# Optimization experiments

Hardware: AMD Instinct MI355X
Metric: run time of the kernel (lower is better)

## Reference

```python
import jax, jax.numpy as jnp
import numpy as np

B, T, E, H, V = 128, 400, 128, 128, 50000
H2, H4, H6 = 2 * H, 4 * H, 6 * H


def setup_inputs() -> dict:
    key = jax.random.key(0)
    ks = jax.random.split(key, 16)
    s = 0.05
    return dict(
        input_ids=jax.random.randint(ks[0], (B, 1), 0, V),
        pre_hidden=jax.random.normal(ks[1], (1, B, H2), jnp.float32),
        pre_cell=jax.random.normal(ks[2], (1, B, H2), jnp.float32),
        enc_outputs=jax.random.normal(ks[3], (B, T, H2), jnp.float32),
        source_input=jax.random.randint(ks[4], (B, T), 0, V),
        coverage=jax.random.uniform(ks[5], (B, 1, T), jnp.float32),
        emb_table=s * jax.random.normal(ks[6], (V, E), jnp.float32),
        w_ih=s * jax.random.normal(ks[7], (4 * H2, E), jnp.float32),
        w_hh=s * jax.random.normal(ks[8], (4 * H2, H2), jnp.float32),
        b_ih=jnp.zeros((4 * H2,), jnp.float32),
        b_hh=jnp.zeros((4 * H2,), jnp.float32),
        w_align=s * jax.random.normal(ks[9], (1, H6), jnp.float32),
        b_align=jnp.zeros((1,), jnp.float32),
        w_cov=s * jax.random.normal(ks[10], (H2, 1), jnp.float32),
        b_cov=jnp.zeros((H2,), jnp.float32),
        w_fc1=s * jax.random.normal(ks[11], (H4, H4), jnp.float32),
        b_fc1=jnp.zeros((H4,), jnp.float32),
        w_fc2=s * jax.random.normal(ks[12], (V, H4), jnp.float32),
        b_fc2=jnp.zeros((V,), jnp.float32),
        w_gen=s * jax.random.normal(ks[13], (1, H4 + E), jnp.float32),
        b_gen=jnp.zeros((1,), jnp.float32),
    )


def reference(input_ids, pre_hidden, pre_cell, enc_outputs, source_input, coverage,
              emb_table, w_ih, w_hh, b_ih, b_hh, w_align, b_align, w_cov, b_cov,
              w_fc1, b_fc1, w_fc2, b_fc2, w_gen, b_gen):
    # embedding lookup (flag=False path: no dropout)
    emb = emb_table[input_ids[:, 0]]                      # [B,E]
    # single-step LSTM (PyTorch gate order i,f,g,o; hidden size 2H)
    h0, c0 = pre_hidden[0], pre_cell[0]                   # [B,2H]
    gates = emb @ w_ih.T + b_ih + h0 @ w_hh.T + b_hh      # [B,8H]
    i, f, g, o = jnp.split(gates, 4, axis=-1)
    c = jax.nn.sigmoid(f) * c0 + jax.nn.sigmoid(i) * jnp.tanh(g)
    h = jax.nn.sigmoid(o) * jnp.tanh(c)                   # [B,2H]
    # coverage feature + attention over encoder steps
    cov_feat = coverage.transpose(0, 2, 1) @ w_cov.T + b_cov        # [B,T,2H]
    h_rep = jnp.broadcast_to(h[:, None, :], enc_outputs.shape)     # [B,T,2H]
    combine = jnp.concatenate([enc_outputs, h_rep, cov_feat], -1)  # [B,T,6H]
    scores = jnp.tanh(combine @ w_align.T + b_align)               # [B,T,1]
    attn = jax.nn.softmax(scores, axis=1)                          # [B,T,1]
    attn_bt = attn[:, :, 0]                                        # [B,T]
    cov_bt = coverage[:, 0, :]
    cov_loss = jnp.sum(jnp.minimum(attn_bt, cov_bt))
    new_cov = coverage + attn_bt[:, None, :]                       # [B,1,T]
    # context + vocab distribution
    context = jnp.einsum('bt,bte->be', attn_bt, enc_outputs)       # [B,2H]
    fc = jnp.tanh(jnp.concatenate([h, context], -1) @ w_fc1.T + b_fc1)
    pvocab = jax.nn.softmax(fc @ w_fc2.T + b_fc2, axis=1)          # [B,V]
    # copy distribution: fused batched scatter-add (replaces per-batch one-hot matmul loop)
    b_idx = jnp.arange(attn_bt.shape[0])[:, None]
    copy = jnp.zeros_like(pvocab).at[b_idx, source_input].add(attn_bt)
    # generation probability and mixture
    gen_in = jnp.concatenate([context, h, emb], -1)                # [B,4H+E]
    pgen = jax.nn.sigmoid(gen_in @ w_gen.T + b_gen)                # [B,1]
    out = pvocab * pgen + copy * (1.0 - pgen)
    return (out, h[None], c[None], attn_bt[:, None, :], copy, new_cov, cov_loss)
```

## Files before the change

kernel.cpp:

```cpp
#include <hip/hip_runtime.h>
#include <hip/hip_bf16.h>
#include <math.h>

#define B_  128
#define T_  400
#define E_  128
#define H2_ 256
#define H4_ 512
#define V_  50000
#define G4_ 1024
#define KACT 384

#define OFF_H       6400000
#define OFF_C       6432768
#define OFF_ATTN    6465536
#define OFF_COPY    6516736
#define OFF_NEWCOV 12916736
#define OFF_COVLOSS 12967936

#define WS_ACT   0
#define WS_GATES (WS_ACT + KACT*B_)
#define WS_HC    (WS_GATES + G4_*B_)
#define WS_FCB   (WS_HC + H4_*B_)
#define WS_SC    (WS_FCB + H4_*B_/2)
#define WS_ATTN  (WS_SC + B_*T_)
#define WS_CTXP  (WS_ATTN + B_*T_)
#define WS_SMP   (WS_CTXP + B_*8*H2_)
#define WS_HDOT  (WS_SMP + B_*8*2)
#define WS_COVP  (WS_HDOT + B_)
#define WS_PGEN  (WS_COVP + B_)
#define WS_MAX   (WS_PGEN + B_)
#define WS_INV   (WS_MAX + B_)
#define WS_AB    (WS_INV + B_)

typedef __attribute__((ext_vector_type(8))) short bf16x8;
typedef __attribute__((ext_vector_type(4))) float f32x4;
typedef __attribute__((ext_vector_type(16))) float f32x16;

__device__ inline float sigmoidf_(float x){ return 1.f/(1.f+__expf(-x)); }

__device__ inline short f2bf(float x){
  __hip_bfloat16 h = __float2bfloat16(x);
  return *reinterpret_cast<short*>(&h);
}

__device__ inline float blk_reduce_sum(float v, float* red){
  int t = threadIdx.x;
  red[t] = v; __syncthreads();
  for (int s = 128; s > 0; s >>= 1){ if (t < s) red[t] += red[t+s]; __syncthreads(); }
  float r = red[0]; __syncthreads(); return r;
}
__device__ inline float blk_reduce_max(float v, float* red){
  int t = threadIdx.x;
  red[t] = v; __syncthreads();
  for (int s = 128; s > 0; s >>= 1){ if (t < s) red[t] = fmaxf(red[t], red[t+s]); __syncthreads(); }
  float r = red[0]; __syncthreads(); return r;
}

__global__ __launch_bounds__(256) void k_zero(float* __restrict__ p){
  size_t i = ((size_t)blockIdx.x*256 + threadIdx.x)*4;
  if (i < (size_t)B_*V_)
    *(float4*)&p[i] = make_float4(0.f,0.f,0.f,0.f);
}

__global__ __launch_bounds__(256) void k_act(const int* __restrict__ ids,
    const float* __restrict__ pre_h, const float* __restrict__ emb_table,
    const float* __restrict__ w_align, const float* __restrict__ w_cov,
    const float* __restrict__ b_cov, float* __restrict__ act,
    float* __restrict__ ab){
  __shared__ float red[256];
  int t = threadIdx.x;
  int idx = blockIdx.x*256 + t;
  int k = idx >> 7, b = idx & 127;
  float v = (k < E_) ? emb_table[(size_t)ids[b]*E_ + k]
                     : pre_h[b*H2_ + (k - E_)];
  act[idx] = v;
  if (blockIdx.x == 0) {
    float wa = w_align[2*H2_ + t];
    float alpha = blk_reduce_sum(w_cov[t]*wa, red);
    float beta  = blk_reduce_sum(b_cov[t]*wa, red);
    if (t == 0) { ab[0] = alpha; ab[1] = beta; }
  }
}

__global__ __launch_bounds__(256) void k_gates(const float* __restrict__ act,
    const float* __restrict__ w_ih, const float* __restrict__ w_hh,
    const float* __restrict__ b_ih, const float* __restrict__ b_hh,
    float* __restrict__ gates){
  __shared__ float wt[8][KACT];
  int t = threadIdx.x; int j0 = blockIdx.x*8;
  for (int idx = t; idx < 8*KACT; idx += 256) {
    int r = idx / KACT, k = idx % KACT;
    int j = j0 + r;
    wt[r][k] = (k < E_) ? w_ih[j*E_ + k] : w_hh[j*H2_ + (k - E_)];
  }
  __syncthreads();
  int jq = t >> 7, b = t & 127;
  float acc[4] = {0.f,0.f,0.f,0.f};
  for (int k = 0; k < KACT; ++k) {
    float a = act[k*B_ + b];
    #pragma unroll
    for (int jj = 0; jj < 4; ++jj) acc[jj] += wt[jq*4+jj][k]*a;
  }
  #pragma unroll
  for (int jj = 0; jj < 4; ++jj) {
    int j = j0 + jq*4 + jj;
    gates[j*B_ + b] = acc[jj] + b_ih[j] + b_hh[j];
  }
}

__global__ __launch_bounds__(256) void k_lstm(const float* __restrict__ gates,
    const float* __restrict__ pre_c, const float* __restrict__ w_align,
    float* __restrict__ o_h, float* __restrict__ o_c,
    float* __restrict__ hc, float* __restrict__ hdot){
  __shared__ float red[256];
  int b = blockIdx.x, k = threadIdx.x;
  float i_ = gates[(0*H2_ + k)*B_ + b];
  float f_ = gates[(1*H2_ + k)*B_ + b];
  float g_ = gates[(2*H2_ + k)*B_ + b];
  float o_ = gates[(3*H2_ + k)*B_ + b];
  float c = sigmoidf_(f_)*pre_c[b*H2_ + k] + sigmoidf_(i_)*tanhf(g_);
  float h = sigmoidf_(o_)*tanhf(c);
  o_h[b*H2_ + k] = h;
  o_c[b*H2_ + k] = c;
  hc[k*B_ + b] = h;
  float s = blk_reduce_sum(h * w_align[H2_ + k], red);
  if (k == 0) hdot[b] = s;
}

__global__ __launch_bounds__(256) void k_scores(const float* __restrict__ enc,
    const float* __restrict__ cov, const float* __restrict__ w_align,
    const float* __restrict__ b_align, const float* __restrict__ hdot,
    const float* __restrict__ ab, float* __restrict__ sc){
  int b = blockIdx.y, c = blockIdx.x;
  int t = threadIdx.x, wave = t >> 6, lane = t & 63;
  float4 wa4 = *(const float4*)&w_align[lane*4];
  float hd = hdot[b], alpha = ab[0], beta = ab[1], ba = b_align[0];
  int t0 = c*50;
  for (int tt = t0 + wave; tt < t0 + 50; tt += 4) {
    const float4* ep = (const float4*)&enc[((size_t)b*T_ + tt)*H2_];
    float4 e4 = ep[lane];
    float d = e4.x*wa4.x + e4.y*wa4.y + e4.z*wa4.z + e4.w*wa4.w;
    #pragma unroll
    for (int m = 32; m >= 1; m >>= 1) d += __shfl_xor(d, m);
    if (lane == 0)
      sc[b*T_ + tt] = tanhf(d + hd + alpha*cov[b*T_ + tt] + beta + ba);
  }
}

__global__ __launch_bounds__(256) void k_soft(const float* __restrict__ sc_in,
    const float* __restrict__ cov, const int* __restrict__ src,
    float* __restrict__ o_attn, float* __restrict__ o_newcov,
    float* __restrict__ o_copy, float* __restrict__ covp,
    float* __restrict__ attn_ws){
  __shared__ float red[256];
  int b = blockIdx.x, t = threadIdx.x;
  float x1 = sc_in[b*T_ + t];
  float x2 = (t + 256 < T_) ? sc_in[b*T_ + t + 256] : -1e30f;
  float mx = blk_reduce_max(fmaxf(x1, x2), red);
  float e1 = __expf(x1 - mx);
  float e2 = (t + 256 < T_) ? __expf(x2 - mx) : 0.f;
  float sum = blk_reduce_sum(e1 + e2, red);
  float inv = 1.f/sum;
  float cl;
  {
    float a1 = e1*inv; float c1 = cov[b*T_ + t];
    attn_ws[b*T_ + t] = a1;
    o_attn[b*T_ + t] = a1;
    o_newcov[b*T_ + t] = c1 + a1;
    atomicAdd(&o_copy[(size_t)b*V_ + src[b*T_ + t]], a1);
    cl = fminf(a1, c1);
  }
  if (t + 256 < T_) {
    float a2 = e2*inv; float c2 = cov[b*T_ + t + 256];
    attn_ws[b*T_ + t + 256] = a2;
    o_attn[b*T_ + t + 256] = a2;
    o_newcov[b*T_ + t + 256] = c2 + a2;
    atomicAdd(&o_copy[(size_t)b*V_ + src[b*T_ + t + 256]], a2);
    cl += fminf(a2, c2);
  }
  float clsum = blk_reduce_sum(cl, red);
  if (t == 0) covp[b] = clsum;
}

__global__ __launch_bounds__(256) void k_ctx(const float* __restrict__ enc,
    const float* __restrict__ attn_ws, float* __restrict__ ctxp){
  __shared__ float a_s[50];
  int b = blockIdx.y, c = blockIdx.x, e = threadIdx.x;
  int t0 = c*50;
  if (e < 50) a_s[e] = attn_ws[b*T_ + t0 + e];
  __syncthreads();
  float acc = 0.f;
  #pragma unroll 5
  for (int i = 0; i < 50; ++i)
    acc += a_s[i] * enc[((size_t)b*T_ + t0 + i)*H2_ + e];
  ctxp[((size_t)b*8 + c)*H2_ + e] = acc;
}

__global__ __launch_bounds__(256) void k_ctxpgen(const float* __restrict__ ctxp,
    const int* __restrict__ ids, const float* __restrict__ emb_table,
    const float* __restrict__ w_gen, const float* __restrict__ b_gen,
    float* __restrict__ hc, float* __restrict__ pgen){
  __shared__ float red[256];
  int b = blockIdx.x, t = threadIdx.x;
  float ctx = 0.f;
  #pragma unroll
  for (int c = 0; c < 8; ++c) ctx += ctxp[((size_t)b*8 + c)*H2_ + t];
  hc[(H2_ + t)*B_ + b] = ctx;
  float p = ctx*w_gen[t] + hc[t*B_ + b]*w_gen[H2_ + t];
  if (t < E_) p += emb_table[(size_t)ids[b]*E_ + t]*w_gen[2*H2_ + t];
  float s = blk_reduce_sum(p, red);
  if (t == 0) pgen[b] = sigmoidf_(s + b_gen[0]);
}

__global__ __launch_bounds__(256) void k_fc1(const float* __restrict__ hc,
    const float* __restrict__ w_fc1, const float* __restrict__ b_fc1,
    short* __restrict__ fcb){
  __shared__ float wt[16][H4_];
  int t = threadIdx.x; int j0 = blockIdx.x*16;
  for (int idx = t; idx < 16*H4_; idx += 256) {
    int r = idx >> 9, k = idx & 511;
    wt[r][k] = w_fc1[(j0 + r)*H4_ + k];
  }
  __syncthreads();
  int jq = t >> 7, b = t & 127;
  float acc[8] = {};
  for (int k = 0; k < H4_; ++k) {
    float a = hc[k*B_ + b];
    #pragma unroll
    for (int jj = 0; jj < 8; ++jj) acc[jj] += wt[jq*8+jj][k]*a;
  }
  bf16x8 pack;
  #pragma unroll
  for (int jj = 0; jj < 8; ++jj) {
    int j = j0 + jq*8 + jj;
    pack[jj] = f2bf(tanhf(acc[jj] + b_fc1[j]));
  }
  *(bf16x8*)&fcb[(size_t)b*H4_ + j0 + jq*8] = pack;
}

#define KH 256
__global__ __launch_bounds__(256, 2) void k_gemm2m(const short* __restrict__ fcb,
    const float* __restrict__ w_fc2, const float* __restrict__ b_fc2,
    float* __restrict__ logits){
  __shared__ short lds[B_*KH];
  char* ldsb = (char*)lds;
  int t = threadIdx.x;
  int w = t >> 6, l = t & 63;
  int ln = l & 31, g2 = l >> 5;
  int v = blockIdx.x*128 + w*32 + ln;
  int vc = v < V_ ? v : V_ - 1;
  f32x16 acc0 = {}, acc1 = {}, acc2 = {}, acc3 = {};

  #pragma unroll
  for (int h = 0; h < 2; ++h) {
    int kb = h*KH;
    if (h) __syncthreads();
    #pragma unroll
    for (int r = 0; r < 16; ++r) {
      int lid = r*256 + t;
      int row = lid >> 5, cg = lid & 31;
      bf16x8 d = *(const bf16x8*)&fcb[row*H4_ + kb + cg*8];
      *(bf16x8*)(ldsb + row*512 + ((cg*16) ^ ((row & 7) << 4))) = d;
    }
    __syncthreads();

    const float* wrow = w_fc2 + (size_t)vc*H4_ + kb + g2*8;
    float4 a0,b0,a1,b1,a2,b2,a3,b3;
    #define LW(s, i) { a##s = *(const float4*)(wrow + (i)*16); \
                       b##s = *(const float4*)(wrow + (i)*16 + 4); }
    #define STEP(s, i)                                                        \
    {                                                                         \
      bf16x8 bf;                                                              \
      bf[0]=f2bf(a##s.x); bf[1]=f2bf(a##s.y); bf[2]=f2bf(a##s.z);             \
      bf[3]=f2bf(a##s.w); bf[4]=f2bf(b##s.x); bf[5]=f2bf(b##s.y);             \
      bf[6]=f2bf(b##s.z); bf[7]=f2bf(b##s.w);                                 \
      int kbyte = (i)*32 + g2*16;                                             \
      { int row = ln;                                                         \
        bf16x8 af = *(const bf16x8*)(ldsb + row*512 + (kbyte ^ ((row&7)<<4)));\
        acc0 = __builtin_amdgcn_mfma_f32_32x32x16_bf16(af, bf, acc0, 0,0,0); }\
      { int row = 32 + ln;                                                    \
        bf16x8 af = *(const bf16x8*)(ldsb + row*512 + (kbyte ^ ((row&7)<<4)));\
        acc1 = __builtin_amdgcn_mfma_f32_32x32x16_bf16(af, bf, acc1, 0,0,0); }\
      { int row = 64 + ln;                                                    \
        bf16x8 af = *(const bf16x8*)(ldsb + row*512 + (kbyte ^ ((row&7)<<4)));\
        acc2 = __builtin_amdgcn_mfma_f32_32x32x16_bf16(af, bf, acc2, 0,0,0); }\
      { int row = 96 + ln;                                                    \
        bf16x8 af = *(const bf16x8*)(ldsb + row*512 + (kbyte ^ ((row&7)<<4)));\
        acc3 = __builtin_amdgcn_mfma_f32_32x32x16_bf16(af, bf, acc3, 0,0,0); }\
    }
    LW(0,0) LW(1,1) LW(2,2) LW(3,3)
    STEP(0,0)  LW(0,4)
    STEP(1,1)  LW(1,5)
    STEP(2,2)  LW(2,6)
    STEP(3,3)  LW(3,7)
    STEP(0,4)  LW(0,8)
    STEP(1,5)  LW(1,9)
    STEP(2,6)  LW(2,10)
    STEP(3,7)  LW(3,11)
    STEP(0,8)  LW(0,12)
    STEP(1,9)  LW(1,13)
    STEP(2,10) LW(2,14)
    STEP(3,11) LW(3,15)
    STEP(0,12)
    STEP(1,13)
    STEP(2,14)
    STEP(3,15)
    #undef LW
    #undef STEP
  }

  if (v < V_) {
    float bias = b_fc2[v];
    #pragma unroll
    for (int r = 0; r < 16; ++r) {
      int brow = (r & 3) + 8*(r >> 2) + 4*g2;
      logits[(size_t)(brow)*V_ + v]      = acc0[r] + bias;
      logits[(size_t)(32 + brow)*V_ + v] = acc1[r] + bias;
      logits[(size_t)(64 + brow)*V_ + v] = acc2[r] + bias;
      logits[(size_t)(96 + brow)*V_ + v] = acc3[r] + bias;
    }
  }
}

__global__ __launch_bounds__(256) void k_smp(const float* __restrict__ logits,
    float* __restrict__ smp){
  __shared__ float rm[256], rs[256];
  int b = blockIdx.y, c = blockIdx.x, t = threadIdx.x;
  int v0 = c*6250, v1 = v0 + 6250;
  float m = -1e30f, s = 0.f;
  for (int v = v0 + t; v < v1; v += 256) {
    float x = logits[(size_t)b*V_ + v];
    float nm = fmaxf(m, x);
    s = s*__expf(m - nm) + __expf(x - nm);
    m = nm;
  }
  rm[t] = m; rs[t] = s; __syncthreads();
  for (int k = 128; k > 0; k >>= 1) {
    if (t < k) {
      float m1 = rm[t], s1 = rs[t], m2 = rm[t+k], s2 = rs[t+k];
      float nm = fmaxf(m1, m2);
      rm[t] = nm; rs[t] = s1*__expf(m1-nm) + s2*__expf(m2-nm);
    }
    __syncthreads();
  }
  if (t == 0) { smp[(b*8+c)*2] = rm[0]; smp[(b*8+c)*2+1] = rs[0]; }
}

__global__ __launch_bounds__(128) void k_smred_cl(const float* __restrict__ smp,
    const float* __restrict__ covp, float* __restrict__ mx,
    float* __restrict__ inv, float* __restrict__ o_cl){
  __shared__ float red[128];
  int t = threadIdx.x;
  float m = -1e30f, s = 0.f;
  #pragma unroll
  for (int c = 0; c < 8; ++c) {
    float m2 = smp[(t*8+c)*2], s2 = smp[(t*8+c)*2+1];
    float nm = fmaxf(m, m2);
    s = s*__expf(m - nm) + s2*__expf(m2 - nm);
    m = nm;
  }
  mx[t] = m; inv[t] = 1.f/s;
  red[t] = covp[t]; __syncthreads();
  for (int k = 64; k > 0; k >>= 1){ if (t < k) red[t] += red[t+k]; __syncthreads(); }
  if (t == 0) o_cl[0] = red[0];
}

__global__ __launch_bounds__(256) void k_final(const float* __restrict__ copy,
    const float* __restrict__ mx, const float* __restrict__ inv_s,
    const float* __restrict__ pgen, float* __restrict__ out){
  size_t gid = (size_t)blockIdx.x*256 + threadIdx.x;
  int b = (int)(gid / (V_/4));
  int v = (int)(gid % (V_/4))*4;
  size_t idx = (size_t)b*V_ + v;
  float m = mx[b], is = inv_s[b], pg = pgen[b];
  float4 lg = *(const float4*)&out[idx];
  float4 cp = *(const float4*)&copy[idx];
  float4 o;
  o.x = __expf(lg.x - m)*is*pg + cp.x*(1.f - pg);
  o.y = __expf(lg.y - m)*is*pg + cp.y*(1.f - pg);
  o.z = __expf(lg.z - m)*is*pg + cp.z*(1.f - pg);
  o.w = __expf(lg.w - m)*is*pg + cp.w*(1.f - pg);
  *(float4*)&out[idx] = o;
}

extern "C" void kernel_launch(void* const* d_in, const int* in_sizes, int n_in,
                              void* d_out, int out_size, void* d_ws, size_t ws_size,
                              hipStream_t stream) {
  const int*   ids       = (const int*)  d_in[0];
  const float* pre_h     = (const float*)d_in[1];
  const float* pre_c     = (const float*)d_in[2];
  const float* enc       = (const float*)d_in[3];
  const int*   src       = (const int*)  d_in[4];
  const float* cov       = (const float*)d_in[5];
  const float* emb_table = (const float*)d_in[6];
  const float* w_ih      = (const float*)d_in[7];
  const float* w_hh      = (const float*)d_in[8];
  const float* b_ih      = (const float*)d_in[9];
  const float* b_hh      = (const float*)d_in[10];
  const float* w_align   = (const float*)d_in[11];
  const float* b_align   = (const float*)d_in[12];
  const float* w_cov     = (const float*)d_in[13];
  const float* b_cov     = (const float*)d_in[14];
  const float* w_fc1     = (const float*)d_in[15];
  const float* b_fc1     = (const float*)d_in[16];
  const float* w_fc2     = (const float*)d_in[17];
  const float* b_fc2     = (const float*)d_in[18];
  const float* w_gen     = (const float*)d_in[19];
  const float* b_gen     = (const float*)d_in[20];

  float* out = (float*)d_out;
  float* ws  = (float*)d_ws;

  float* o_out    = out;
  float* o_h      = out + OFF_H;
  float* o_c      = out + OFF_C;
  float* o_attn   = out + OFF_ATTN;
  float* o_copy   = out + OFF_COPY;
  float* o_newcov = out + OFF_NEWCOV;
  float* o_cl     = out + OFF_COVLOSS;

  k_zero <<<(B_*V_/4 + 255)/256, 256, 0, stream>>>(o_copy);
  k_act  <<<192, 256, 0, stream>>>(ids, pre_h, emb_table, w_align, w_cov, b_cov,
                                   ws + WS_ACT, ws + WS_AB);
  k_gates<<<128, 256, 0, stream>>>(ws + WS_ACT, w_ih, w_hh, b_ih, b_hh, ws + WS_GATES);
  k_lstm <<<128, 256, 0, stream>>>(ws + WS_GATES, pre_c, w_align, o_h, o_c,
                                   ws + WS_HC, ws + WS_HDOT);
  k_scores<<<dim3(8,128), 256, 0, stream>>>(enc, cov, w_align, b_align,
                                   ws + WS_HDOT, ws + WS_AB, ws + WS_SC);
  k_soft <<<128, 256, 0, stream>>>(ws + WS_SC, cov, src, o_attn, o_newcov, o_copy,
                                   ws + WS_COVP, ws + WS_ATTN);
  k_ctx  <<<dim3(8,128), 256, 0, stream>>>(enc, ws + WS_ATTN, ws + WS_CTXP);
  k_ctxpgen<<<128, 256, 0, stream>>>(ws + WS_CTXP, ids, emb_table, w_gen, b_gen,
                                   ws + WS_HC, ws + WS_PGEN);
  k_fc1  <<<32, 256, 0, stream>>>(ws + WS_HC, w_fc1, b_fc1, (short*)(ws + WS_FCB));
  k_gemm2m<<<(V_ + 127)/128, 256, 0, stream>>>((const short*)(ws + WS_FCB),
                                   w_fc2, b_fc2, o_out);
  k_smp  <<<dim3(8,128), 256, 0, stream>>>(o_out, ws + WS_SMP);
  k_smred_cl<<<1, 128, 0, stream>>>(ws + WS_SMP, ws + WS_COVP,
                                   ws + WS_MAX, ws + WS_INV, o_cl);
  k_final<<<(int)(((size_t)B_*V_/4)/256), 256, 0, stream>>>(
      o_copy, ws + WS_MAX, ws + WS_INV, ws + WS_PGEN, o_out);
}
```

Before: 149.7 us.

## Split fc2 GEMM over K into two partial-sum blocks, reduce in softmax pass

```diff
diff --git a/kernel.cpp b/kernel.cpp
--- a/kernel.cpp
+++ b/kernel.cpp
@@ -32,6 +32,8 @@
 #define WS_MAX   (WS_PGEN + B_)
 #define WS_INV   (WS_MAX + B_)
 #define WS_AB    (WS_INV + B_)
+#define WS_P0    (WS_AB + 16)
+#define WS_P1    (WS_P0 + B_*V_)
 
 typedef __attribute__((ext_vector_type(8))) short bf16x8;
 typedef __attribute__((ext_vector_type(4))) float f32x4;
@@ -239,100 +241,107 @@
   *(bf16x8*)&fcb[(size_t)b*H4_ + j0 + jq*8] = pack;
 }
 
-#define KH 256
+#define KSH 256
 __global__ __launch_bounds__(256, 2) void k_gemm2m(const short* __restrict__ fcb,
-    const float* __restrict__ w_fc2, const float* __restrict__ b_fc2,
-    float* __restrict__ logits){
-  __shared__ short lds[B_*KH];
+    const float* __restrict__ w_fc2, float* __restrict__ part){
+  __shared__ short lds[B_*KSH];
   char* ldsb = (char*)lds;
   int t = threadIdx.x;
+  int half = blockIdx.x & 1;
+  int vt = blockIdx.x >> 1;
+  int kb = half * KSH;
   int w = t >> 6, l = t & 63;
   int ln = l & 31, g2 = l >> 5;
-  int v = blockIdx.x*128 + w*32 + ln;
+  int v = vt*128 + w*32 + ln;
   int vc = v < V_ ? v : V_ - 1;
+
+  #pragma unroll
+  for (int r = 0; r < 16; ++r) {
+    int lid = r*256 + t;
+    int row = lid >> 5, cg = lid & 31;
+    bf16x8 d = *(const bf16x8*)&fcb[row*H4_ + kb + cg*8];
+    *(bf16x8*)(ldsb + row*512 + ((cg*16) ^ ((row & 31) << 4))) = d;
+  }
+
+  const float* wrow = w_fc2 + (size_t)vc*H4_ + kb + g2*8;
   f32x16 acc0 = {}, acc1 = {}, acc2 = {}, acc3 = {};
 
-  #pragma unroll
-  for (int h = 0; h < 2; ++h) {
-    int kb = h*KH;
-    if (h) __syncthreads();
-    #pragma unroll
-    for (int r = 0; r < 16; ++r) {
-      int lid = r*256 + t;
-      int row = lid >> 5, cg = lid & 31;
-      bf16x8 d = *(const bf16x8*)&fcb[row*H4_ + kb + cg*8];
-      *(bf16x8*)(ldsb + row*512 + ((cg*16) ^ ((row & 7) << 4))) = d;
-    }
-    __syncthreads();
-
-    const float* wrow = w_fc2 + (size_t)vc*H4_ + kb + g2*8;
-    float4 a0,b0,a1,b1,a2,b2,a3,b3;
-    #define LW(s, i) { a##s = *(const float4*)(wrow + (i)*16); \
-                       b##s = *(const float4*)(wrow + (i)*16 + 4); }
-    #define STEP(s, i)                                                        \
-    {                                                                         \
-      bf16x8 bf;                                                              \
-      bf[0]=f2bf(a##s.x); bf[1]=f2bf(a##s.y); bf[2]=f2bf(a##s.z);             \
-      bf[3]=f2bf(a##s.w); bf[4]=f2bf(b##s.x); bf[5]=f2bf(b##s.y);             \
-      bf[6]=f2bf(b##s.z); bf[7]=f2bf(b##s.w);                                 \
-      int kbyte = (i)*32 + g2*16;                                             \
-      { int row = ln;                                                         \
-        bf16x8 af = *(const bf16x8*)(ldsb + row*512 + (kbyte ^ ((row&7)<<4)));\
-        acc0 = __builtin_amdgcn_mfma_f32_32x32x16_bf16(af, bf, acc0, 0,0,0); }\
-      { int row = 32 + ln;                                                    \
-        bf16x8 af = *(const bf16x8*)(ldsb + row*512 + (kbyte ^ ((row&7)<<4)));\
-        acc1 = __builtin_amdgcn_mfma_f32_32x32x16_bf16(af, bf, acc1, 0,0,0); }\
-      { int row = 64 + ln;                                                    \
-        bf16x8 af = *(const bf16x8*)(ldsb + row*512 + (kbyte ^ ((row&7)<<4)));\
-        acc2 = __builtin_amdgcn_mfma_f32_32x32x16_bf16(af, bf, acc2, 0,0,0); }\
-      { int row = 96 + ln;                                                    \
-        bf16x8 af = *(const bf16x8*)(ldsb + row*512 + (kbyte ^ ((row&7)<<4)));\
-        acc3 = __builtin_amdgcn_mfma_f32_32x32x16_bf16(af, bf, acc3, 0,0,0); }\
-    }
-    LW(0,0) LW(1,1) LW(2,2) LW(3,3)
-    STEP(0,0)  LW(0,4)
-    STEP(1,1)  LW(1,5)
-    STEP(2,2)  LW(2,6)
-    STEP(3,3)  LW(3,7)
-    STEP(0,4)  LW(0,8)
-    STEP(1,5)  LW(1,9)
-    STEP(2,6)  LW(2,10)
-    STEP(3,7)  LW(3,11)
-    STEP(0,8)  LW(0,12)
-    STEP(1,9)  LW(1,13)
-    STEP(2,10) LW(2,14)
-    STEP(3,11) LW(3,15)
-    STEP(0,12)
-    STEP(1,13)
-    STEP(2,14)
-    STEP(3,15)
-    #undef LW
-    #undef STEP
-  }
+  #define LDQ(nm, s) float4 nm##a = *(const float4*)(wrow + (s)*16); \
+                     float4 nm##b = *(const float4*)(wrow + (s)*16 + 4);
+  #define STEPX(nm, s)                                                        \
+  {                                                                           \
+    bf16x8 bf;                                                                \
+    bf[0]=f2bf(nm##a.x); bf[1]=f2bf(nm##a.y); bf[2]=f2bf(nm##a.z);            \
+    bf[3]=f2bf(nm##a.w); bf[4]=f2bf(nm##b.x); bf[5]=f2bf(nm##b.y);            \
+    bf[6]=f2bf(nm##b.z); bf[7]=f2bf(nm##b.w);                                 \
+    int kbyte = (s)*32 + g2*16;                                               \
+    { int row = ln;                                                           \
+      bf16x8 af = *(const bf16x8*)(ldsb + row*512 + (kbyte ^ ((row&31)<<4))); \
+      acc0 = __builtin_amdgcn_mfma_f32_32x32x16_bf16(af, bf, acc0, 0,0,0); }  \
+    { int row = 32 + ln;                                                      \
+      bf16x8 af = *(const bf16x8*)(ldsb + row*512 + (kbyte ^ ((row&31)<<4))); \
+      acc1 = __builtin_amdgcn_mfma_f32_32x32x16_bf16(af, bf, acc1, 0,0,0); }  \
+    { int row = 64 + ln;                                                      \
+      bf16x8 af = *(const bf16x8*)(ldsb + row*512 + (kbyte ^ ((row&31)<<4))); \
+      acc2 = __builtin_amdgcn_mfma_f32_32x32x16_bf16(af, bf, acc2, 0,0,0); }  \
+    { int row = 96 + ln;                                                      \
+      bf16x8 af = *(const bf16x8*)(ldsb + row*512 + (kbyte ^ ((row&31)<<4))); \
+      acc3 = __builtin_amdgcn_mfma_f32_32x32x16_bf16(af, bf, acc3, 0,0,0); }  \
+  }
+
+  LDQ(q0,0) LDQ(q1,1) LDQ(q2,2) LDQ(q3,3)
+  LDQ(q4,4) LDQ(q5,5) LDQ(q6,6) LDQ(q7,7)
+  __syncthreads();
+  LDQ(r0,8)   STEPX(q0,0)
+  LDQ(r1,9)   STEPX(q1,1)
+  LDQ(r2,10)  STEPX(q2,2)
+  LDQ(r3,11)  STEPX(q3,3)
+  LDQ(r4,12)  STEPX(q4,4)
+  LDQ(r5,13)  STEPX(q5,5)
+  LDQ(r6,14)  STEPX(q6,6)
+  LDQ(r7,15)  STEPX(q7,7)
+  STEPX(r0,8)
+  STEPX(r1,9)
+  STEPX(r2,10)
+  STEPX(r3,11)
+  STEPX(r4,12)
+  STEPX(r5,13)
+  STEPX(r6,14)
+  STEPX(r7,15)
+  #undef LDQ
+  #undef STEPX
 
   if (v < V_) {
-    float bias = b_fc2[v];
+    float* pp = part + (size_t)half*B_*V_;
     #pragma unroll
     for (int r = 0; r < 16; ++r) {
       int brow = (r & 3) + 8*(r >> 2) + 4*g2;
-      logits[(size_t)(brow)*V_ + v]      = acc0[r] + bias;
-      logits[(size_t)(32 + brow)*V_ + v] = acc1[r] + bias;
-      logits[(size_t)(64 + brow)*V_ + v] = acc2[r] + bias;
-      logits[(size_t)(96 + brow)*V_ + v] = acc3[r] + bias;
+      pp[(size_t)(brow)*V_ + v]      = acc0[r];
+      pp[(size_t)(32 + brow)*V_ + v] = acc1[r];
+      pp[(size_t)(64 + brow)*V_ + v] = acc2[r];
+      pp[(size_t)(96 + brow)*V_ + v] = acc3[r];
     }
   }
 }
 
-__global__ __launch_bounds__(256) void k_smp(const float* __restrict__ logits,
-    float* __restrict__ smp){
+__global__ __launch_bounds__(256) void k_smp(const float* __restrict__ p0,
+    const float* __restrict__ p1, const float* __restrict__ b_fc2,
+    float* __restrict__ logits, float* __restrict__ smp){
   __shared__ float rm[256], rs[256];
   int b = blockIdx.y, c = blockIdx.x, t = threadIdx.x;
   int v0 = c*6250, v1 = v0 + 6250;
+  size_t base = (size_t)b*V_;
   float m = -1e30f, s = 0.f;
-  for (int v = v0 + t; v < v1; v += 256) {
-    float x = logits[(size_t)b*V_ + v];
-    float nm = fmaxf(m, x);
-    s = s*__expf(m - nm) + __expf(x - nm);
+  for (int v = v0 + t*2; v < v1; v += 512) {
+    float2 a0 = *(const float2*)&p0[base + v];
+    float2 a1 = *(const float2*)&p1[base + v];
+    float2 bb = *(const float2*)&b_fc2[v];
+    float2 x;
+    x.x = a0.x + a1.x + bb.x;
+    x.y = a0.y + a1.y + bb.y;
+    *(float2*)&logits[base + v] = x;
+    float nm = fmaxf(m, fmaxf(x.x, x.y));
+    s = s*__expf(m - nm) + __expf(x.x - nm) + __expf(x.y - nm);
     m = nm;
   }
   rm[t] = m; rs[t] = s; __syncthreads();
@@ -434,9 +443,10 @@
   k_ctxpgen<<<128, 256, 0, stream>>>(ws + WS_CTXP, ids, emb_table, w_gen, b_gen,
                                    ws + WS_HC, ws + WS_PGEN);
   k_fc1  <<<32, 256, 0, stream>>>(ws + WS_HC, w_fc1, b_fc1, (short*)(ws + WS_FCB));
-  k_gemm2m<<<(V_ + 127)/128, 256, 0, stream>>>((const short*)(ws + WS_FCB),
-                                   w_fc2, b_fc2, o_out);
-  k_smp  <<<dim3(8,128), 256, 0, stream>>>(o_out, ws + WS_SMP);
+  k_gemm2m<<<2*((V_ + 127)/128), 256, 0, stream>>>((const short*)(ws + WS_FCB),
+                                   w_fc2, ws + WS_P0);
+  k_smp  <<<dim3(8,128), 256, 0, stream>>>(ws + WS_P0, ws + WS_P1, b_fc2,
+                                   o_out, ws + WS_SMP);
   k_smred_cl<<<1, 128, 0, stream>>>(ws + WS_SMP, ws + WS_COVP,
                                    ws + WS_MAX, ws + WS_INV, o_cl);
   k_final<<<(int)(((size_t)B_*V_/4)/256), 256, 0, stream>>>(
```

Result: slower. 165.0 us (+10.2%).
